# Kernel tuning notes

Hardware: AMD Instinct MI355X
Metric: run time of the kernel (lower is better)

## Reference

```python
import jax, jax.numpy as jnp
import numpy as np

N_HEAD = 8
EPS = 1e-6  # LayerNorm2d eps


def setup_inputs() -> dict:
    key = jax.random.key(0)
    ks = jax.random.split(key, 7)
    B, C, H, W = 16, 256, 128, 128
    nh, dk, dv = N_HEAD, 32, 32
    s = 1.0 / np.sqrt(C)
    return {
        "q": jax.random.normal(ks[0], (B, C, H, W), jnp.float32),
        "k": jax.random.normal(ks[1], (B, C, H, W), jnp.float32),
        "v": jax.random.normal(ks[2], (B, C, H, W), jnp.float32),
        # 1x1 convs without bias == channel matmuls; weight shape [out_ch, in_ch]
        "wq": jax.random.normal(ks[3], (nh * dk, C), jnp.float32) * s,
        "wk": jax.random.normal(ks[4], (nh * dk, C), jnp.float32) * s,
        "wv": jax.random.normal(ks[5], (nh * dv, C), jnp.float32) * s,
        "wfc": jax.random.normal(ks[6], (C, nh * dv), jnp.float32) * (1.0 / np.sqrt(nh * dv)),
        "ln_w": jnp.ones((C,), jnp.float32),
        "ln_b": jnp.zeros((C,), jnp.float32),
        "kernel": 5,
        "pad": 2,
    }


def _forward(q, k, v, wq, wk, wv, wfc, ln_w, ln_b, kernel, pad):
    B, C, H, W = q.shape
    nh = N_HEAD
    dk = wq.shape[0] // nh
    dv = wv.shape[0] // nh
    assert kernel == 2 * pad + 1
    residual = q
    # 1x1 conv projections, split into heads: [B, nh, d, H, W]
    qh = jnp.einsum('oc,bchw->bohw', wq, q).reshape(B, nh, dk, H, W)
    kh = jnp.einsum('oc,bchw->bohw', wk, k).reshape(B, nh, dk, H, W)
    vh = jnp.einsum('oc,bchw->bohw', wv, v).reshape(B, nh, dv, H, W)
    # zero-pad spatially: out-of-bounds correlations/values are zero, matching the
    # original bilinear sampler (zeros padding) and the custom padding() helper.
    kp = jnp.pad(kh, ((0, 0), (0, 0), (0, 0), (pad, pad), (pad, pad)))
    vp = jnp.pad(vh, ((0, 0), (0, 0), (0, 0), (pad, pad), (pad, pad)))
    # local correlation volume: dot(q[i,j], k[i+dy-pad, j+dx-pad]) for the KxK window
    # (integer offsets -> bilinear sample degenerates to a gather). Never materializes
    # the full [B, HW, HW] matrix the torch code builds before sampling.
    corr = jnp.stack(
        [jnp.einsum('bncij,bncij->bnij', qh, kp[:, :, :, dy:dy + H, dx:dx + W])
         for dy in range(kernel) for dx in range(kernel)], axis=-1)  # [B,nh,H,W,K*K]
    # relu (from CorrBlock.corr), temperature = sqrt(d_k), softmax over window.
    # OOB entries are 0 (not -inf), faithfully matching the original.
    attn = jax.nn.softmax(jax.nn.relu(corr) / jnp.float32(np.sqrt(dk)), axis=-1)
    # channel attention: per-pixel weighted sum of v over the same window
    out = jnp.zeros((B, nh, dv, H, W), q.dtype)
    idx = 0
    for dy in range(kernel):
        for dx in range(kernel):
            out = out + attn[:, :, :, :, idx][:, :, None] * vp[:, :, :, dy:dy + H, dx:dx + W]
            idx += 1
    o = jnp.einsum('oc,bchw->bohw', wfc, out.reshape(B, nh * dv, H, W)) + residual
    # LayerNorm2d: normalize over channel dim per pixel
    mu = o.mean(1, keepdims=True)
    var = ((o - mu) ** 2).mean(1, keepdims=True)
    y = (o - mu) / jnp.sqrt(var + EPS)
    return ln_w[None, :, None, None] * y + ln_b[None, :, None, None]


def reference(q, k, v, wq, wk, wv, wfc, ln_w, ln_b, kernel, pad):
    return _forward(q, k, v, wq, wk, wv, wfc, ln_w, ln_b, kernel, pad)
```

## Files before the change

### kernel.cpp

```cpp
#include <hip/hip_runtime.h>
#include <hip/hip_bf16.h>

#define BATCH 16
#define CH 256
#define HH 128
#define WW 128
#define HWSZ (HH * WW)
#define NHEAD 8
#define DHEAD 32
#define PW 132
#define PPIX (132 * 132)
#define ROWS 264

typedef __attribute__((ext_vector_type(8))) short bf16x8;
typedef __attribute__((ext_vector_type(4))) float f32x4;
typedef _Float16 h2v __attribute__((ext_vector_type(2)));

__device__ __forceinline__ unsigned short f2h(float f) {
    _Float16 h = (_Float16)f;
    return __builtin_bit_cast(unsigned short, h);
}
__device__ __forceinline__ unsigned pkbf(float a, float b) {
    __hip_bfloat162_raw r = __hip_bfloat162_raw(__float22bfloat162_rn(make_float2(a, b)));
    return (unsigned)r.x | ((unsigned)r.y << 16);
}

#if __has_builtin(__builtin_amdgcn_fdot2)
#define DOT2(a, b, c) __builtin_amdgcn_fdot2((a), (b), (c), false)
#else
#define DOT2(a, b, c) ((c) + (float)(a)[0] * (float)(b)[0] + (float)(a)[1] * (float)(b)[1])
#endif

__global__ __launch_bounds__(256)
void zpad_kernel(unsigned short* __restrict__ kpad, unsigned short* __restrict__ vpad)
{
    int bid = blockIdx.x;
    unsigned short* dst = ((bid & 1) ? vpad : kpad) + (size_t)(bid >> 1) * PPIX * DHEAD;
    const uint4 z = {0u, 0u, 0u, 0u};
    for (int i = threadIdx.x; i < 1040; i += 256) {
        int row, col;
        if (i < 264)      { row = i / 132; col = i - row * 132; }
        else if (i < 528) { int j = i - 264; int r = j / 132; row = 130 + r; col = j - r * 132; }
        else              { int j = i - 528; row = 2 + (j >> 2); int c = j & 3; col = (c < 2) ? c : (128 + c); }
        uint4* p = reinterpret_cast<uint4*>(dst + (size_t)(row * PW + col) * DHEAD);
        p[0] = z; p[1] = z; p[2] = z; p[3] = z;
    }
}

__global__ __launch_bounds__(256)
void prep_kernel(const float* __restrict__ wq, const float* __restrict__ wk,
                 const float* __restrict__ wv, const float* __restrict__ wfc,
                 unsigned short* __restrict__ wb)
{
    const float* src = (blockIdx.y == 0) ? wq : (blockIdx.y == 1) ? wk
                     : (blockIdx.y == 2) ? wv : wfc;
    unsigned short* dst = wb + blockIdx.y * 65536;
    int e = (blockIdx.x * 256 + threadIdx.x) * 8;
    const float4* s = reinterpret_cast<const float4*>(src + e);
    float4 a = s[0], c = s[1];
    uint4 u;
    u.x = pkbf(a.x, a.y); u.y = pkbf(a.z, a.w);
    u.z = pkbf(c.x, c.y); u.w = pkbf(c.z, c.w);
    *reinterpret_cast<uint4*>(dst + e) = u;
}

__global__ __launch_bounds__(256)
void proj_kernel(const float* __restrict__ q, const float* __restrict__ k,
                 const float* __restrict__ v, const unsigned short* __restrict__ wb,
                 unsigned short* __restrict__ qh, unsigned short* __restrict__ kpad,
                 unsigned short* __restrict__ vpad)
{
    __shared__ __align__(16) unsigned short lB[64 * ROWS];

    const int t = threadIdx.x;
    const int b = blockIdx.y;
    const int p0 = blockIdx.x * 64;
    const int z = blockIdx.z;

    const float* X; unsigned short* Y;
    if (z == 0)      { X = q; Y = qh; }
    else if (z == 1) { X = k; Y = kpad; }
    else             { X = v; Y = vpad; }
    const unsigned short* Wb = wb + z * 65536;
    X += (size_t)b * CH * HWSZ;
    const size_t pixstride = (z == 0) ? (size_t)HWSZ : (size_t)PPIX;
    Y += (size_t)b * NHEAD * pixstride * DHEAD;

    const int lane = t & 63;
    const int wid  = t >> 6;
    const int lrow = lane & 15;
    const int lkg  = lane >> 4;
    const int pB   = t & 63;
    const int cg   = t >> 6;

#pragma unroll
    for (int i = 0; i < 8; ++i) {
        const float* xp = X + (size_t)((cg * 8 + i) * 8) * HWSZ + p0 + pB;
        float fv[8];
#pragma unroll
        for (int j = 0; j < 8; ++j) fv[j] = xp[(size_t)j * HWSZ];
        uint4 u;
        u.x = pkbf(fv[0], fv[1]); u.y = pkbf(fv[2], fv[3]);
        u.z = pkbf(fv[4], fv[5]); u.w = pkbf(fv[6], fv[7]);
        *reinterpret_cast<uint4*>(&lB[pB * ROWS + (cg * 8 + i) * 8]) = u;
    }

    bf16x8 afc[4], afn[4];
#pragma unroll
    for (int m = 0; m < 4; ++m)
        afc[m] = *reinterpret_cast<const bf16x8*>(Wb + (wid * 64 + m * 16 + lrow) * 256 + lkg * 8);

    f32x4 acc[4][4];
    const f32x4 zero = {0.f, 0.f, 0.f, 0.f};
#pragma unroll
    for (int m = 0; m < 4; ++m)
#pragma unroll
        for (int n = 0; n < 4; ++n) acc[m][n] = zero;

    __syncthreads();

#pragma unroll
    for (int ks = 0; ks < 8; ++ks) {
        if (ks < 7) {
#pragma unroll
            for (int m = 0; m < 4; ++m)
                afn[m] = *reinterpret_cast<const bf16x8*>(Wb + (wid * 64 + m * 16 + lrow) * 256 + (ks + 1) * 32 + lkg * 8);
        }
        bf16x8 bfv[4];
#pragma unroll
        for (int n = 0; n < 4; ++n)
            bfv[n] = *reinterpret_cast<const bf16x8*>(&lB[(n * 16 + lrow) * ROWS + (ks * 4 + lkg) * 8]);
#pragma unroll
        for (int m = 0; m < 4; ++m)
#pragma unroll
            for (int n = 0; n < 4; ++n)
                acc[m][n] = __builtin_amdgcn_mfma_f32_16x16x32_bf16(afc[m], bfv[n], acc[m][n], 0, 0, 0);
#pragma unroll
        for (int m = 0; m < 4; ++m) afc[m] = afn[m];
    }

    const int lr = lane >> 4, lc = lane & 15;
#pragma unroll
    for (int m = 0; m < 4; ++m)
#pragma unroll
        for (int n = 0; n < 4; ++n) {
            int o = wid * 64 + m * 16 + lr * 4;
            int hh_ = o >> 5, d0 = o & 31;
            int p = p0 + n * 16 + lc;
            ushort4 pk;
            pk.x = f2h(acc[m][n][0]); pk.y = f2h(acc[m][n][1]);
            pk.z = f2h(acc[m][n][2]); pk.w = f2h(acc[m][n][3]);
            size_t pix;
            if (z == 0) pix = (size_t)hh_ * HWSZ + p;
            else { int row = p >> 7, col = p & 127; pix = (size_t)hh_ * PPIX + (size_t)(row + 2) * PW + (col + 2); }
            *reinterpret_cast<ushort4*>(&Y[pix * DHEAD + d0]) = pk;
        }
}

__global__ __launch_bounds__(1024)
void attn_kernel(unsigned short* __restrict__ qh,
                 const unsigned short* __restrict__ kpad,
                 const unsigned short* __restrict__ vpad)
{
    const int t = threadIdx.x;
    const int swz = (blockIdx.x & 7) * 1024 + (blockIdx.x >> 3);
    const int bh = swz >> 6;
    const int tile = swz & 63;
    const int x0 = (tile & 7) * 16, y0 = (tile >> 3) * 16;
    const int qc = t & 3;
    const int px = (t >> 2) & 15;
    const int py = t >> 6;
    const int gx = x0 + px, gy = y0 + py;

    unsigned short* qp = qh + ((size_t)bh * HWSZ + gy * WW + gx) * DHEAD + qc * 8;
    const unsigned short* kb = kpad + (size_t)bh * PPIX * DHEAD + qc * 8;
    const unsigned short* vb = vpad + (size_t)bh * PPIX * DHEAD + qc * 8;

    union { uint4 u; h2v h2[4]; } Q;
    Q.u = *reinterpret_cast<const uint4*>(qp);

    float ew[25];
#pragma unroll
    for (int wy = 0; wy < 5; ++wy) {
        const unsigned short* krow = kb + (size_t)((gy + wy) * PW + gx) * DHEAD;
#pragma unroll
        for (int wx = 0; wx < 5; ++wx) {
            union { uint4 u; h2v h2[4]; } K;
            K.u = *reinterpret_cast<const uint4*>(krow + wx * DHEAD);
            float s = 0.f;
#pragma unroll
            for (int j = 0; j < 4; ++j)
                s = DOT2(Q.h2[j], K.h2[j], s);
            s += __shfl_xor(s, 1);
            s += __shfl_xor(s, 2);
            ew[wy * 5 + wx] = __expf(fmaxf(s, 0.f) * 0.17677669529663687f);
        }
    }

    float sum = 0.f;
#pragma unroll
    for (int i = 0; i < 25; ++i) sum += ew[i];
    const float inv = 1.f / sum;

    union { uint4 u; h2v h2[4]; } A;
    const h2v hz = {(_Float16)0.f, (_Float16)0.f};
#pragma unroll
    for (int j = 0; j < 4; ++j) A.h2[j] = hz;

#pragma unroll
    for (int wy = 0; wy < 5; ++wy) {
        const unsigned short* vrow = vb + (size_t)((gy + wy) * PW + gx) * DHEAD;
#pragma unroll
        for (int wx = 0; wx < 5; ++wx) {
            _Float16 wh = (_Float16)(ew[wy * 5 + wx] * inv);
            h2v w2 = {wh, wh};
            union { uint4 u; h2v h2[4]; } V;
            V.u = *reinterpret_cast<const uint4*>(vrow + wx * DHEAD);
#pragma unroll
            for (int j = 0; j < 4; ++j)
                A.h2[j] += w2 * V.h2[j];
        }
    }

    uint4 o;
    o.x = pkbf((float)A.h2[0][0], (float)A.h2[0][1]);
    o.y = pkbf((float)A.h2[1][0], (float)A.h2[1][1]);
    o.z = pkbf((float)A.h2[2][0], (float)A.h2[2][1]);
    o.w = pkbf((float)A.h2[3][0], (float)A.h2[3][1]);
    *reinterpret_cast<uint4*>(qp) = o;
}

__global__ __launch_bounds__(256)
void fcln_kernel(const unsigned short* __restrict__ ob, const unsigned short* __restrict__ wfcb,
                 const float* __restrict__ qres, const float* __restrict__ lnw,
                 const float* __restrict__ lnb, float* __restrict__ out)
{
    __shared__ __align__(16) unsigned short lB[64 * ROWS];
    __shared__ float lsum[4][64];
    __shared__ float lssq[4][64];

    const int t = threadIdx.x;
    const int b = blockIdx.y;
    const int p0 = blockIdx.x * 64;

    const int lane = t & 63;
    const int wid  = t >> 6;
    const int lrow = lane & 15;
    const int lkg  = lane >> 4;
    const int pxf  = t >> 2;
    const int qcf  = t & 3;

#pragma unroll
    for (int h = 0; h < 8; ++h) {
        uint4 bv = *reinterpret_cast<const uint4*>(
            ob + ((size_t)(b * NHEAD + h) * HWSZ + p0 + pxf) * DHEAD + qcf * 8);
        *reinterpret_cast<uint4*>(&lB[pxf * ROWS + (h * 4 + qcf) * 8]) = bv;
    }

    bf16x8 afc[4], afn[4];
#pragma unroll
    for (int m = 0; m < 4; ++m)
        afc[m] = *reinterpret_cast<const bf16x8*>(wfcb + (wid * 64 + m * 16 + lrow) * 256 + lkg * 8);

    f32x4 acc[4][4];
    const f32x4 zero = {0.f, 0.f, 0.f, 0.f};
#pragma unroll
    for (int m = 0; m < 4; ++m)
#pragma unroll
        for (int n = 0; n < 4; ++n) acc[m][n] = zero;

    __syncthreads();

#pragma unroll
    for (int ks = 0; ks < 8; ++ks) {
        if (ks < 7) {
#pragma unroll
            for (int m = 0; m < 4; ++m)
                afn[m] = *reinterpret_cast<const bf16x8*>(wfcb + (wid * 64 + m * 16 + lrow) * 256 + (ks + 1) * 32 + lkg * 8);
        }
        bf16x8 bfv[4];
#pragma unroll
        for (int n = 0; n < 4; ++n)
            bfv[n] = *reinterpret_cast<const bf16x8*>(&lB[(n * 16 + lrow) * ROWS + (ks * 4 + lkg) * 8]);
#pragma unroll
        for (int m = 0; m < 4; ++m)
#pragma unroll
            for (int n = 0; n < 4; ++n)
                acc[m][n] = __builtin_amdgcn_mfma_f32_16x16x32_bf16(afc[m], bfv[n], acc[m][n], 0, 0, 0);
#pragma unroll
        for (int m = 0; m < 4; ++m) afc[m] = afn[m];
    }

    const int lr = lane >> 4, lc = lane & 15;
    const float* qb = qres + (size_t)b * CH * HWSZ;
#pragma unroll
    for (int m = 0; m < 4; ++m)
#pragma unroll
        for (int n = 0; n < 4; ++n)
#pragma unroll
            for (int j = 0; j < 4; ++j) {
                int o = wid * 64 + m * 16 + lr * 4 + j;
                int p = p0 + n * 16 + lc;
                acc[m][n][j] += qb[(size_t)o * HWSZ + p];
            }

    float s[4], s2[4];
#pragma unroll
    for (int n = 0; n < 4; ++n) {
        float a = 0.f, c2 = 0.f;
#pragma unroll
        for (int m = 0; m < 4; ++m)
#pragma unroll
            for (int j = 0; j < 4; ++j) {
                float x = acc[m][n][j];
                a += x; c2 += x * x;
            }
        a  += __shfl_xor(a, 16);  a  += __shfl_xor(a, 32);
        c2 += __shfl_xor(c2, 16); c2 += __shfl_xor(c2, 32);
        s[n] = a; s2[n] = c2;
    }
    if (lane < 16) {
#pragma unroll
        for (int n = 0; n < 4; ++n) {
            lsum[wid][n * 16 + lane] = s[n];
            lssq[wid][n * 16 + lane] = s2[n];
        }
    }
    __syncthreads();

    float mu[4], rs[4];
#pragma unroll
    for (int n = 0; n < 4; ++n) {
        int p = n * 16 + lc;
        float ts = lsum[0][p] + lsum[1][p] + lsum[2][p] + lsum[3][p];
        float tq = lssq[0][p] + lssq[1][p] + lssq[2][p] + lssq[3][p];
        float m_ = ts * (1.f / 256.f);
        float v_ = tq * (1.f / 256.f) - m_ * m_;
        mu[n] = m_;
        rs[n] = rsqrtf(v_ + 1e-6f);
    }

    float* op = out + (size_t)b * CH * HWSZ;
#pragma unroll
    for (int m = 0; m < 4; ++m)
#pragma unroll
        for (int j = 0; j < 4; ++j) {
            int o = wid * 64 + m * 16 + lr * 4 + j;
            float g = lnw[o], bb = lnb[o];
#pragma unroll
            for (int n = 0; n < 4; ++n) {
                int p = p0 + n * 16 + lc;
                op[(size_t)o * HWSZ + p] = (acc[m][n][j] - mu[n]) * rs[n] * g + bb;
            }
        }
}

extern "C" void kernel_launch(void* const* d_in, const int* in_sizes, int n_in,
                              void* d_out, int out_size, void* d_ws, size_t ws_size,
                              hipStream_t stream) {
    const float* q   = (const float*)d_in[0];
    const float* k   = (const float*)d_in[1];
    const float* v   = (const float*)d_in[2];
    const float* wq  = (const float*)d_in[3];
    const float* wk  = (const float*)d_in[4];
    const float* wv  = (const float*)d_in[5];
    const float* wfc = (const float*)d_in[6];
    const float* lnw = (const float*)d_in[7];
    const float* lnb = (const float*)d_in[8];

    const size_t qsz = (size_t)BATCH * NHEAD * HWSZ * DHEAD;
    const size_t psz = (size_t)BATCH * NHEAD * PPIX * DHEAD;
    if (ws_size < (qsz + 2 * psz + 4 * 65536) * sizeof(unsigned short)) return;

    unsigned short* qh = (unsigned short*)d_ws;
    unsigned short* kp = qh + qsz;
    unsigned short* vp = kp + psz;
    unsigned short* wb = vp + psz;

    zpad_kernel<<<256, 256, 0, stream>>>(kp, vp);
    prep_kernel<<<dim3(32, 4), 256, 0, stream>>>(wq, wk, wv, wfc, wb);
    proj_kernel<<<dim3(HWSZ / 64, BATCH, 3), 256, 0, stream>>>(q, k, v, wb, qh, kp, vp);
    attn_kernel<<<8192, 1024, 0, stream>>>(qh, kp, vp);
    fcln_kernel<<<dim3(HWSZ / 64, BATCH), 256, 0, stream>>>(qh, wb + 3 * 65536, q, lnw, lnb, (float*)d_out);
}
```

Measured before the change: 776.5 us.

## Use 512-thread blocks with XOR-swizzled LDS in projection and fc/LayerNorm GEMMs

Doubles the block size of the projection and output-fc/LayerNorm kernels to 8 waves, so each wave owns 32 output channels instead of 64. All global loads are issued before the LDS writes, with a scheduling barrier in between to batch memory requests. LDS tiles gain an XOR swizzle keyed on pixel row to reduce bank conflicts on the MFMA B-operand reads. The LayerNorm reduction now covers 8 waves. The aim is more waves and more memory parallelism per block in these bandwidth-bound GEMMs, at the cost of more weight-fragment reloads per block and a larger cross-wave reduction.

```diff
diff --git a/kernel.cpp b/kernel.cpp
--- a/kernel.cpp
+++ b/kernel.cpp
@@ -64,7 +64,7 @@
     *reinterpret_cast<uint4*>(dst + e) = u;
 }
 
-__global__ __launch_bounds__(256)
+__global__ __launch_bounds__(512)
 void proj_kernel(const float* __restrict__ q, const float* __restrict__ k,
                  const float* __restrict__ v, const unsigned short* __restrict__ wb,
                  unsigned short* __restrict__ qh, unsigned short* __restrict__ kpad,
@@ -92,28 +92,32 @@
     const int lkg  = lane >> 4;
     const int pB   = t & 63;
     const int cg   = t >> 6;
-
-#pragma unroll
-    for (int i = 0; i < 8; ++i) {
-        const float* xp = X + (size_t)((cg * 8 + i) * 8) * HWSZ + p0 + pB;
-        float fv[8];
-#pragma unroll
-        for (int j = 0; j < 8; ++j) fv[j] = xp[(size_t)j * HWSZ];
+    const int psw  = pB >> 3;
+
+    float fv[32];
+    {
+        const float* xb = X + p0 + pB + (size_t)(cg * 32) * HWSZ;
+#pragma unroll
+        for (int i = 0; i < 32; ++i) fv[i] = xb[(size_t)i * HWSZ];
+    }
+    __builtin_amdgcn_sched_barrier(0);
+#pragma unroll
+    for (int i = 0; i < 4; ++i) {
         uint4 u;
-        u.x = pkbf(fv[0], fv[1]); u.y = pkbf(fv[2], fv[3]);
-        u.z = pkbf(fv[4], fv[5]); u.w = pkbf(fv[6], fv[7]);
-        *reinterpret_cast<uint4*>(&lB[pB * ROWS + (cg * 8 + i) * 8]) = u;
-    }
-
-    bf16x8 afc[4], afn[4];
-#pragma unroll
-    for (int m = 0; m < 4; ++m)
-        afc[m] = *reinterpret_cast<const bf16x8*>(Wb + (wid * 64 + m * 16 + lrow) * 256 + lkg * 8);
-
-    f32x4 acc[4][4];
+        u.x = pkbf(fv[i*8+0], fv[i*8+1]); u.y = pkbf(fv[i*8+2], fv[i*8+3]);
+        u.z = pkbf(fv[i*8+4], fv[i*8+5]); u.w = pkbf(fv[i*8+6], fv[i*8+7]);
+        *reinterpret_cast<uint4*>(&lB[pB * ROWS + ((cg * 4 + i) ^ psw) * 8]) = u;
+    }
+
+    bf16x8 afc[2], afn[2];
+#pragma unroll
+    for (int m = 0; m < 2; ++m)
+        afc[m] = *reinterpret_cast<const bf16x8*>(Wb + (wid * 32 + m * 16 + lrow) * 256 + lkg * 8);
+
+    f32x4 acc[2][4];
     const f32x4 zero = {0.f, 0.f, 0.f, 0.f};
 #pragma unroll
-    for (int m = 0; m < 4; ++m)
+    for (int m = 0; m < 2; ++m)
 #pragma unroll
         for (int n = 0; n < 4; ++n) acc[m][n] = zero;
 
@@ -123,36 +127,37 @@
     for (int ks = 0; ks < 8; ++ks) {
         if (ks < 7) {
 #pragma unroll
-            for (int m = 0; m < 4; ++m)
-                afn[m] = *reinterpret_cast<const bf16x8*>(Wb + (wid * 64 + m * 16 + lrow) * 256 + (ks + 1) * 32 + lkg * 8);
+            for (int m = 0; m < 2; ++m)
+                afn[m] = *reinterpret_cast<const bf16x8*>(Wb + (wid * 32 + m * 16 + lrow) * 256 + (ks + 1) * 32 + lkg * 8);
         }
         bf16x8 bfv[4];
 #pragma unroll
-        for (int n = 0; n < 4; ++n)
-            bfv[n] = *reinterpret_cast<const bf16x8*>(&lB[(n * 16 + lrow) * ROWS + (ks * 4 + lkg) * 8]);
-#pragma unroll
-        for (int m = 0; m < 4; ++m)
+        for (int n = 0; n < 4; ++n) {
+            int row = n * 16 + lrow;
+            bfv[n] = *reinterpret_cast<const bf16x8*>(&lB[row * ROWS + ((ks * 4 + lkg) ^ (row >> 3)) * 8]);
+        }
+#pragma unroll
+        for (int m = 0; m < 2; ++m)
 #pragma unroll
             for (int n = 0; n < 4; ++n)
                 acc[m][n] = __builtin_amdgcn_mfma_f32_16x16x32_bf16(afc[m], bfv[n], acc[m][n], 0, 0, 0);
 #pragma unroll
-        for (int m = 0; m < 4; ++m) afc[m] = afn[m];
+        for (int m = 0; m < 2; ++m) afc[m] = afn[m];
     }
 
     const int lr = lane >> 4, lc = lane & 15;
 #pragma unroll
-    for (int m = 0; m < 4; ++m)
+    for (int m = 0; m < 2; ++m)
 #pragma unroll
         for (int n = 0; n < 4; ++n) {
-            int o = wid * 64 + m * 16 + lr * 4;
-            int hh_ = o >> 5, d0 = o & 31;
+            int d0 = m * 16 + lr * 4;
             int p = p0 + n * 16 + lc;
             ushort4 pk;
             pk.x = f2h(acc[m][n][0]); pk.y = f2h(acc[m][n][1]);
             pk.z = f2h(acc[m][n][2]); pk.w = f2h(acc[m][n][3]);
             size_t pix;
-            if (z == 0) pix = (size_t)hh_ * HWSZ + p;
-            else { int row = p >> 7, col = p & 127; pix = (size_t)hh_ * PPIX + (size_t)(row + 2) * PW + (col + 2); }
+            if (z == 0) pix = (size_t)wid * HWSZ + p;
+            else { int row = p >> 7, col = p & 127; pix = (size_t)wid * PPIX + (size_t)(row + 2) * PW + (col + 2); }
             *reinterpret_cast<ushort4*>(&Y[pix * DHEAD + d0]) = pk;
         }
 }
@@ -230,14 +235,14 @@
     *reinterpret_cast<uint4*>(qp) = o;
 }
 
-__global__ __launch_bounds__(256)
+__global__ __launch_bounds__(512)
 void fcln_kernel(const unsigned short* __restrict__ ob, const unsigned short* __restrict__ wfcb,
                  const float* __restrict__ qres, const float* __restrict__ lnw,
                  const float* __restrict__ lnb, float* __restrict__ out)
 {
     __shared__ __align__(16) unsigned short lB[64 * ROWS];
-    __shared__ float lsum[4][64];
-    __shared__ float lssq[4][64];
+    __shared__ float lsum[8][64];
+    __shared__ float lssq[8][64];
 
     const int t = threadIdx.x;
     const int b = blockIdx.y;
@@ -247,25 +252,36 @@
     const int wid  = t >> 6;
     const int lrow = lane & 15;
     const int lkg  = lane >> 4;
-    const int pxf  = t >> 2;
-    const int qcf  = t & 3;
-
-#pragma unroll
-    for (int h = 0; h < 8; ++h) {
-        uint4 bv = *reinterpret_cast<const uint4*>(
-            ob + ((size_t)(b * NHEAD + h) * HWSZ + p0 + pxf) * DHEAD + qcf * 8);
-        *reinterpret_cast<uint4*>(&lB[pxf * ROWS + (h * 4 + qcf) * 8]) = bv;
-    }
-
-    bf16x8 afc[4], afn[4];
-#pragma unroll
-    for (int m = 0; m < 4; ++m)
-        afc[m] = *reinterpret_cast<const bf16x8*>(wfcb + (wid * 64 + m * 16 + lrow) * 256 + lkg * 8);
-
-    f32x4 acc[4][4];
+
+    uint4 bv[4];
+#pragma unroll
+    for (int r = 0; r < 4; ++r) {
+        int idx = r * 512 + t;
+        int h  = idx >> 8;
+        int rem = idx & 255;
+        int px = rem >> 2, qc = rem & 3;
+        bv[r] = *reinterpret_cast<const uint4*>(
+            ob + ((size_t)(b * NHEAD + h) * HWSZ + p0 + px) * DHEAD + qc * 8);
+    }
+    __builtin_amdgcn_sched_barrier(0);
+#pragma unroll
+    for (int r = 0; r < 4; ++r) {
+        int idx = r * 512 + t;
+        int h  = idx >> 8;
+        int rem = idx & 255;
+        int px = rem >> 2, qc = rem & 3;
+        *reinterpret_cast<uint4*>(&lB[px * ROWS + ((h * 4 + qc) ^ (px >> 3)) * 8]) = bv[r];
+    }
+
+    bf16x8 afc[2], afn[2];
+#pragma unroll
+    for (int m = 0; m < 2; ++m)
+        afc[m] = *reinterpret_cast<const bf16x8*>(wfcb + (wid * 32 + m * 16 + lrow) * 256 + lkg * 8);
+
+    f32x4 acc[2][4];
     const f32x4 zero = {0.f, 0.f, 0.f, 0.f};
 #pragma unroll
-    for (int m = 0; m < 4; ++m)
+    for (int m = 0; m < 2; ++m)
 #pragma unroll
         for (int n = 0; n < 4; ++n) acc[m][n] = zero;
 
@@ -275,31 +291,33 @@
     for (int ks = 0; ks < 8; ++ks) {
         if (ks < 7) {
 #pragma unroll
-            for (int m = 0; m < 4; ++m)
-                afn[m] = *reinterpret_cast<const bf16x8*>(wfcb + (wid * 64 + m * 16 + lrow) * 256 + (ks + 1) * 32 + lkg * 8);
+            for (int m = 0; m < 2; ++m)
+                afn[m] = *reinterpret_cast<const bf16x8*>(wfcb + (wid * 32 + m * 16 + lrow) * 256 + (ks + 1) * 32 + lkg * 8);
         }
         bf16x8 bfv[4];
 #pragma unroll
-        for (int n = 0; n < 4; ++n)
-            bfv[n] = *reinterpret_cast<const bf16x8*>(&lB[(n * 16 + lrow) * ROWS + (ks * 4 + lkg) * 8]);
-#pragma unroll
-        for (int m = 0; m < 4; ++m)
+        for (int n = 0; n < 4; ++n) {
+            int row = n * 16 + lrow;
+            bfv[n] = *reinterpret_cast<const bf16x8*>(&lB[row * ROWS + ((ks * 4 + lkg) ^ (row >> 3)) * 8]);
+        }
+#pragma unroll
+        for (int m = 0; m < 2; ++m)
 #pragma unroll
             for (int n = 0; n < 4; ++n)
                 acc[m][n] = __builtin_amdgcn_mfma_f32_16x16x32_bf16(afc[m], bfv[n], acc[m][n], 0, 0, 0);
 #pragma unroll
-        for (int m = 0; m < 4; ++m) afc[m] = afn[m];
+        for (int m = 0; m < 2; ++m) afc[m] = afn[m];
     }
 
     const int lr = lane >> 4, lc = lane & 15;
     const float* qb = qres + (size_t)b * CH * HWSZ;
 #pragma unroll
-    for (int m = 0; m < 4; ++m)
+    for (int m = 0; m < 2; ++m)
 #pragma unroll
         for (int n = 0; n < 4; ++n)
 #pragma unroll
             for (int j = 0; j < 4; ++j) {
-                int o = wid * 64 + m * 16 + lr * 4 + j;
+                int o = wid * 32 + m * 16 + lr * 4 + j;
                 int p = p0 + n * 16 + lc;
                 acc[m][n][j] += qb[(size_t)o * HWSZ + p];
             }
@@ -309,7 +327,7 @@
     for (int n = 0; n < 4; ++n) {
         float a = 0.f, c2 = 0.f;
 #pragma unroll
-        for (int m = 0; m < 4; ++m)
+        for (int m = 0; m < 2; ++m)
 #pragma unroll
             for (int j = 0; j < 4; ++j) {
                 float x = acc[m][n][j];
@@ -332,8 +350,9 @@
 #pragma unroll
     for (int n = 0; n < 4; ++n) {
         int p = n * 16 + lc;
-        float ts = lsum[0][p] + lsum[1][p] + lsum[2][p] + lsum[3][p];
-        float tq = lssq[0][p] + lssq[1][p] + lssq[2][p] + lssq[3][p];
+        float ts = 0.f, tq = 0.f;
+#pragma unroll
+        for (int w = 0; w < 8; ++w) { ts += lsum[w][p]; tq += lssq[w][p]; }
         float m_ = ts * (1.f / 256.f);
         float v_ = tq * (1.f / 256.f) - m_ * m_;
         mu[n] = m_;
@@ -342,10 +361,10 @@
 
     float* op = out + (size_t)b * CH * HWSZ;
 #pragma unroll
-    for (int m = 0; m < 4; ++m)
+    for (int m = 0; m < 2; ++m)
 #pragma unroll
         for (int j = 0; j < 4; ++j) {
-            int o = wid * 64 + m * 16 + lr * 4 + j;
+            int o = wid * 32 + m * 16 + lr * 4 + j;
             float g = lnw[o], bb = lnb[o];
 #pragma unroll
             for (int n = 0; n < 4; ++n) {
@@ -379,7 +398,7 @@
 
     zpad_kernel<<<256, 256, 0, stream>>>(kp, vp);
     prep_kernel<<<dim3(32, 4), 256, 0, stream>>>(wq, wk, wv, wfc, wb);
-    proj_kernel<<<dim3(HWSZ / 64, BATCH, 3), 256, 0, stream>>>(q, k, v, wb, qh, kp, vp);
+    proj_kernel<<<dim3(HWSZ / 64, BATCH, 3), 512, 0, stream>>>(q, k, v, wb, qh, kp, vp);
     attn_kernel<<<8192, 1024, 0, stream>>>(qh, kp, vp);
-    fcln_kernel<<<dim3(HWSZ / 64, BATCH), 256, 0, stream>>>(qh, wb + 3 * 65536, q, lnw, lnb, (float*)d_out);
-}
+    fcln_kernel<<<dim3(HWSZ / 64, BATCH), 512, 0, stream>>>(qh, wb + 3 * 65536, q, lnw, lnb, (float*)d_out);
+}
```

New measurement: 783.7 us. About the same (+0.9%).
